# Optimization experiments

Hardware: AMD Instinct MI355X
Metric: run time of the kernel (lower is better)

## Reference

```python
import jax, jax.numpy as jnp
import numpy as np

NUM_CLASSES = 32
SIGMA = 0.02
LOG_SIGMA = float(np.log(SIGMA))
HALF_LOG_2PI = float(0.5 * np.log(2.0 * np.pi))


def _gcn(x, adj, W1, b1, W2, b2):
    # Two-layer GCN: h = relu(A x W1 + b1); out = A h W2 + b2
    h = jax.nn.relu(jnp.einsum('bij,bjf->bif', adj, x) @ W1 + b1)
    return jnp.einsum('bij,bjf->bif', adj, h) @ W2 + b2


def setup_inputs() -> dict:
    key = jax.random.key(0)
    ks = jax.random.split(key, 10)
    B, N, F = 64, 1024, 512
    x = jax.random.normal(ks[0], (B, N, F), dtype=jnp.float32)
    adj = jax.random.uniform(ks[1], (B, N, N), dtype=jnp.float32) / N  # row-scaled dense adjacency
    masks = jax.random.randint(ks[2], (B, N, F), 0, 2, dtype=jnp.int32)
    noise = jax.random.normal(ks[3], (B, N, F), dtype=jnp.float32)
    s = 0.05
    We1 = jax.random.normal(ks[4], (F, 30), dtype=jnp.float32) * s
    be1 = jnp.zeros((30,), dtype=jnp.float32)
    We2 = jax.random.normal(ks[5], (30, 18), dtype=jnp.float32) * s
    be2 = jnp.zeros((18,), dtype=jnp.float32)
    Wd1 = jax.random.normal(ks[6], (18, 30), dtype=jnp.float32) * s
    bd1 = jnp.zeros((30,), dtype=jnp.float32)
    Wd2 = jax.random.normal(ks[7], (30, F), dtype=jnp.float32) * s
    bd2 = jnp.zeros((F,), dtype=jnp.float32)
    return dict(x=x, adj=adj, masks=masks, noise=noise, We1=We1, be1=be1,
                We2=We2, be2=be2, Wd1=Wd1, bd1=bd1, Wd2=Wd2, bd2=bd2)


def reference(x, adj, masks, noise, We1, be1, We2, be2, Wd1, bd1, Wd2, bd2):
    enc = _gcn(x, adj, We1, be1, We2, be2)            # [B,N,18]
    dec = _gcn(enc, adj, Wd1, bd1, Wd2, bd2)          # [B,N,F]
    dec_act = jnp.concatenate(
        (jax.nn.softmax(dec[..., :NUM_CLASSES], axis=-1),
         jax.nn.sigmoid(dec[..., NUM_CLASSES:])), axis=-1)
    m = masks.astype(dec_act.dtype)
    # Vectorized masked reparameterized Gaussian sample: s = mu + sigma*eps
    sampled = dec_act + m * (SIGMA * noise)
    # log N(s; mu, sigma) = -eps^2/2 - log(sigma) - 0.5*log(2pi), summed over masked entries
    lp_elem = -0.5 * noise * noise - LOG_SIGMA - HALF_LOG_2PI
    log_probs = jnp.sum(m * lp_elem, axis=(1, 2))      # [B]
    return dec, sampled, log_probs
```

## Files before the change

kernel.cpp:

```cpp
#include <hip/hip_runtime.h>

#define B_ 64
#define NN 1024
#define FF 512

typedef float  fx4 __attribute__((ext_vector_type(4)));
typedef float  fx2 __attribute__((ext_vector_type(2)));
typedef int    ix4 __attribute__((ext_vector_type(4)));
typedef unsigned int   ux4i __attribute__((ext_vector_type(4)));
typedef unsigned int   ux2i __attribute__((ext_vector_type(2)));
typedef unsigned short us4  __attribute__((ext_vector_type(4)));
typedef short  sx8 __attribute__((ext_vector_type(8)));

#define FP8_SCALE   16384.0f
#define INV_SCALE   6.103515625e-5f

static __device__ __forceinline__ unsigned short f2bf(float f){
    union { float f; unsigned u; } v; v.f = f;
    unsigned r = v.u + 0x7FFFu + ((v.u >> 16) & 1u);
    return (unsigned short)(r >> 16);
}
static __device__ __forceinline__ float bf2f(unsigned short h){
    union { unsigned u; float f; } v; v.u = ((unsigned)h) << 16;
    return v.f;
}
static __device__ __forceinline__ unsigned cvt_pk_bf16(float lo, float hi){
    unsigned r;
    asm("v_cvt_pk_bf16_f32 %0, %1, %2" : "=v"(r) : "v"(lo), "v"(hi));
    return r;
}
static __device__ __forceinline__ sx8 pack_bf16x8(fx4 v0, fx4 v1){
    union { unsigned u[4]; sx8 s; } r;
    r.u[0] = cvt_pk_bf16(v0[0], v0[1]);
    r.u[1] = cvt_pk_bf16(v0[2], v0[3]);
    r.u[2] = cvt_pk_bf16(v1[0], v1[1]);
    r.u[3] = cvt_pk_bf16(v1[2], v1[3]);
    return r.s;
}
template<typename T>
static __device__ __forceinline__ T ntload(const T* p){ return __builtin_nontemporal_load(p); }
static __device__ __forceinline__ void ntstore4(float* p, fx4 v){
    __builtin_nontemporal_store(v, (fx4*)p);
}

__global__ __launch_bounds__(512) void k_xw1(
    const float* __restrict__ x, const float* __restrict__ We1,
    unsigned short* __restrict__ u1T){
    __shared__ unsigned short wls[32*512];
    int tid = threadIdx.x;
    for (int i = tid; i < 32*512; i += 512){
        int col = i >> 9, k = i & 511;
        float v = (col < 30) ? We1[k*30 + col] : 0.f;
        wls[col*512 + ((((k >> 3) ^ (col & 7)) << 3) | (k & 7))] = f2bf(v);
    }
    __syncthreads();
    int w = tid >> 6, l = tid & 63;
    int lr = l & 15, kq = l >> 4;
    int b = blockIdx.y;
    int rowb = blockIdx.x*128 + w*16;
    const float* xp = x + ((size_t)b*NN + rowb + lr)*FF + kq*8;
    fx4 acc0 = {0,0,0,0}, acc1 = {0,0,0,0};
    int c0 = lr, c1 = 16 + lr;
    #pragma unroll 4
    for (int kk = 0; kk < FF; kk += 32){
        fx4 v0 = ntload((const fx4*)(xp + kk));
        fx4 v1 = ntload((const fx4*)(xp + kk + 4));
        sx8 a = pack_bf16x8(v0, v1);
        int chunk = (kk >> 3) + kq;
        sx8 b0 = *(const sx8*)(wls + c0*512 + ((chunk ^ (c0 & 7)) << 3));
        sx8 b1 = *(const sx8*)(wls + c1*512 + ((chunk ^ (c1 & 7)) << 3));
        acc0 = __builtin_amdgcn_mfma_f32_16x16x32_bf16(a, b0, acc0, 0, 0, 0);
        acc1 = __builtin_amdgcn_mfma_f32_16x16x32_bf16(a, b1, acc1, 0, 0, 0);
    }
    int row0 = rowb + kq*4;
    us4 o0 = { f2bf(acc0[0]), f2bf(acc0[1]), f2bf(acc0[2]), f2bf(acc0[3]) };
    us4 o1 = { f2bf(acc1[0]), f2bf(acc1[1]), f2bf(acc1[2]), f2bf(acc1[3]) };
    *(us4*)(u1T + ((size_t)b*32 + c0)*NN + row0) = o0;
    *(us4*)(u1T + ((size_t)b*32 + c1)*NN + row0) = o1;
}

__global__ __launch_bounds__(256) void k_cvt_h1(
    const float* __restrict__ adjf, unsigned char* __restrict__ adj8,
    const unsigned short* __restrict__ uT, const float* __restrict__ bias,
    unsigned short* __restrict__ outT){
    __shared__ unsigned short uts[32*NN];
    int tid = threadIdx.x;
    int rt = blockIdx.x, b = blockIdx.y;
    const ux4i* src = (const ux4i*)(uT + (size_t)b*32*NN);
    #pragma unroll
    for (int i = 0; i < 16; i++){
        int j = tid + i*256;
        int c = j >> 7;
        ux4i v = src[j];
        int dst = (j*16) ^ ((c & 7) << 4);
        *(ux4i*)((char*)uts + dst) = v;
    }
    __syncthreads();
    int w = tid >> 6, l = tid & 63;
    int lr = l & 15, lk = (l >> 4) * 8;
    size_t aoff = (size_t)b*NN*NN + (size_t)(rt*128 + w*32 + lr)*NN + lk;
    int c0 = lr, c1 = 16 + lr;
    fx4 acc00 = {0,0,0,0}, acc01 = {0,0,0,0}, acc10 = {0,0,0,0}, acc11 = {0,0,0,0};
    #pragma unroll 4
    for (int kk = 0; kk < NN; kk += 32){
        fx4 v00 = ntload((const fx4*)(adjf + aoff + kk));
        fx4 v01 = ntload((const fx4*)(adjf + aoff + kk + 4));
        fx4 v10 = ntload((const fx4*)(adjf + aoff + 16*NN + kk));
        fx4 v11 = ntload((const fx4*)(adjf + aoff + 16*NN + kk + 4));
        sx8 a0 = pack_bf16x8(v00, v01);
        sx8 a1 = pack_bf16x8(v10, v11);
        {
            const float S = FP8_SCALE;
            int d0 = __builtin_amdgcn_cvt_pk_fp8_f32(v00[0]*S, v00[1]*S, 0, false);
            d0     = __builtin_amdgcn_cvt_pk_fp8_f32(v00[2]*S, v00[3]*S, d0, true);
            int d1 = __builtin_amdgcn_cvt_pk_fp8_f32(v01[0]*S, v01[1]*S, 0, false);
            d1     = __builtin_amdgcn_cvt_pk_fp8_f32(v01[2]*S, v01[3]*S, d1, true);
            ux2i s0 = { (unsigned)d0, (unsigned)d1 };
            *(ux2i*)(adj8 + aoff + kk) = s0;
            int d2 = __builtin_amdgcn_cvt_pk_fp8_f32(v10[0]*S, v10[1]*S, 0, false);
            d2     = __builtin_amdgcn_cvt_pk_fp8_f32(v10[2]*S, v10[3]*S, d2, true);
            int d3 = __builtin_amdgcn_cvt_pk_fp8_f32(v11[0]*S, v11[1]*S, 0, false);
            d3     = __builtin_amdgcn_cvt_pk_fp8_f32(v11[2]*S, v11[3]*S, d3, true);
            ux2i s1 = { (unsigned)d2, (unsigned)d3 };
            *(ux2i*)(adj8 + aoff + 16*NN + kk) = s1;
        }
        int kb = (kk + lk) * 2;
        sx8 b0 = *(const sx8*)((const char*)uts + ((c0*2048 + kb) ^ ((c0 & 7) << 4)));
        sx8 b1 = *(const sx8*)((const char*)uts + ((c1*2048 + kb) ^ ((c1 & 7) << 4)));
        acc00 = __builtin_amdgcn_mfma_f32_16x16x32_bf16(a0, b0, acc00, 0, 0, 0);
        acc01 = __builtin_amdgcn_mfma_f32_16x16x32_bf16(a0, b1, acc01, 0, 0, 0);
        acc10 = __builtin_amdgcn_mfma_f32_16x16x32_bf16(a1, b0, acc10, 0, 0, 0);
        acc11 = __builtin_amdgcn_mfma_f32_16x16x32_bf16(a1, b1, acc11, 0, 0, 0);
    }
    float bias0 = (c0 < 30) ? bias[c0] : 0.f;
    float bias1 = 0.f;
    if (c1 < 30) bias1 = bias[c1];
    int lq = l >> 4;
    #pragma unroll
    for (int mt = 0; mt < 2; mt++){
        int row0 = rt*128 + w*32 + mt*16 + lq*4;
        fx4 am0 = mt ? acc10 : acc00;
        fx4 am1 = mt ? acc11 : acc01;
        #pragma unroll
        for (int ct = 0; ct < 2; ct++){
            fx4 a = ct ? am1 : am0;
            float bb = ct ? bias1 : bias0;
            int col = ct ? c1 : c0;
            us4 o;
            #pragma unroll
            for (int j = 0; j < 4; j++){
                float v = fmaxf(a[j] + bb, 0.f);
                o[j] = f2bf(v);
            }
            *(us4*)(outT + ((size_t)b*32 + col)*NN + row0) = o;
        }
    }
}

template<int RM>
__global__ __launch_bounds__(256) void k_adjf8(
    const unsigned char* __restrict__ adj8,
    const unsigned short* __restrict__ uT,
    const float* __restrict__ bias, int biasN, float oscale,
    unsigned short* __restrict__ outT){
    __shared__ unsigned short uts[32*NN];
    int tid = threadIdx.x;
    int rt = blockIdx.x, b = blockIdx.y;
    const ux4i* src = (const ux4i*)(uT + (size_t)b*32*NN);
    #pragma unroll
    for (int i = 0; i < 16; i++){
        int j = tid + i*256;
        int c = j >> 7;
        ux4i v = src[j];
        int dst = (j*16) ^ ((c & 7) << 4);
        *(ux4i*)((char*)uts + dst) = v;
    }
    __syncthreads();
    int w = tid >> 6, l = tid & 63;
    int lr = l & 15, lk = (l >> 4) * 8;
    size_t aoff = (size_t)b*NN*NN + (size_t)(rt*128 + w*32 + lr)*NN + lk;
    int c0 = lr, c1 = 16 + lr;
    fx4 acc00 = {0,0,0,0}, acc01 = {0,0,0,0}, acc10 = {0,0,0,0}, acc11 = {0,0,0,0};
    #pragma unroll 4
    for (int kk = 0; kk < NN; kk += 32){
        ux2i q0 = *(const ux2i*)(adj8 + aoff + kk);
        ux2i q1 = *(const ux2i*)(adj8 + aoff + 16*NN + kk);
        fx2 f0 = __builtin_amdgcn_cvt_pk_f32_fp8((int)q0[0], false);
        fx2 f1 = __builtin_amdgcn_cvt_pk_f32_fp8((int)q0[0], true);
        fx2 f2 = __builtin_amdgcn_cvt_pk_f32_fp8((int)q0[1], false);
        fx2 f3 = __builtin_amdgcn_cvt_pk_f32_fp8((int)q0[1], true);
        fx2 g0 = __builtin_amdgcn_cvt_pk_f32_fp8((int)q1[0], false);
        fx2 g1 = __builtin_amdgcn_cvt_pk_f32_fp8((int)q1[0], true);
        fx2 g2 = __builtin_amdgcn_cvt_pk_f32_fp8((int)q1[1], false);
        fx2 g3 = __builtin_amdgcn_cvt_pk_f32_fp8((int)q1[1], true);
        union { unsigned u[4]; sx8 s; } A0, A1;
        A0.u[0] = cvt_pk_bf16(f0[0], f0[1]);
        A0.u[1] = cvt_pk_bf16(f1[0], f1[1]);
        A0.u[2] = cvt_pk_bf16(f2[0], f2[1]);
        A0.u[3] = cvt_pk_bf16(f3[0], f3[1]);
        A1.u[0] = cvt_pk_bf16(g0[0], g0[1]);
        A1.u[1] = cvt_pk_bf16(g1[0], g1[1]);
        A1.u[2] = cvt_pk_bf16(g2[0], g2[1]);
        A1.u[3] = cvt_pk_bf16(g3[0], g3[1]);
        int kb = (kk + lk) * 2;
        sx8 b0 = *(const sx8*)((const char*)uts + ((c0*2048 + kb) ^ ((c0 & 7) << 4)));
        sx8 b1 = *(const sx8*)((const char*)uts + ((c1*2048 + kb) ^ ((c1 & 7) << 4)));
        acc00 = __builtin_amdgcn_mfma_f32_16x16x32_bf16(A0.s, b0, acc00, 0, 0, 0);
        acc01 = __builtin_amdgcn_mfma_f32_16x16x32_bf16(A0.s, b1, acc01, 0, 0, 0);
        acc10 = __builtin_amdgcn_mfma_f32_16x16x32_bf16(A1.s, b0, acc10, 0, 0, 0);
        acc11 = __builtin_amdgcn_mfma_f32_16x16x32_bf16(A1.s, b1, acc11, 0, 0, 0);
    }
    float bias0 = 0.f, bias1 = 0.f;
    if (bias){
        if (c0 < biasN) bias0 = bias[c0];
        if (c1 < biasN) bias1 = bias[c1];
    }
    int lq = l >> 4;
    #pragma unroll
    for (int mt = 0; mt < 2; mt++){
        int row0 = rt*128 + w*32 + mt*16 + lq*4;
        fx4 am0 = mt ? acc10 : acc00;
        fx4 am1 = mt ? acc11 : acc01;
        #pragma unroll
        for (int ct = 0; ct < 2; ct++){
            fx4 a = ct ? am1 : am0;
            float bb = ct ? bias1 : bias0;
            int col = ct ? c1 : c0;
            us4 o;
            #pragma unroll
            for (int j = 0; j < 4; j++){
                float v = (a[j] + bb) * oscale;
                o[j] = f2bf(v);
            }
            if (RM){
                #pragma unroll
                for (int j = 0; j < 4; j++)
                    outT[((size_t)b*NN + row0 + j)*32 + col] = o[j];
            } else {
                *(us4*)(outT + ((size_t)b*32 + col)*NN + row0) = o;
            }
        }
    }
}

template<int JI, int CO, bool RELU>
__global__ __launch_bounds__(256) void k_tiny(
    const unsigned short* __restrict__ inT, const float* __restrict__ W,
    const float* __restrict__ bias, float oscale,
    unsigned short* __restrict__ outT){
    int n = blockIdx.x*256 + threadIdx.x;
    int b = blockIdx.y;
    const unsigned short* ip = inT + (size_t)b*32*NN + n;
    float in[JI];
    #pragma unroll
    for (int j = 0; j < JI; j++) in[j] = bf2f(ip[j*NN]);
    float acc[CO];
    #pragma unroll
    for (int c = 0; c < CO; c++) acc[c] = bias ? bias[c] : 0.f;
    #pragma unroll
    for (int j = 0; j < JI; j++){
        #pragma unroll
        for (int c = 0; c < CO; c++) acc[c] += in[j] * W[j*CO + c];
    }
    unsigned short* op = outT + (size_t)b*32*NN + n;
    #pragma unroll
    for (int c = 0; c < 32; c++){
        float v = (c < CO) ? (RELU ? fmaxf(acc[c], 0.f) : acc[c]) * oscale : 0.f;
        op[c*NN] = f2bf(v);
    }
}

__global__ __launch_bounds__(512, 2) void k_dec(
    const unsigned short* __restrict__ v2R,
    const float* __restrict__ Wd2, const float* __restrict__ bd2,
    const int* __restrict__ masks, const float* __restrict__ noise,
    float* __restrict__ dec, float* __restrict__ sampled, float* __restrict__ part){
    __shared__ unsigned short wls[512*40];
    __shared__ float dls[16][516];
    __shared__ float red[8];
    int tid = threadIdx.x;
    for (int i = tid; i < 512*32; i += 512){
        int col = i & 511, k = i >> 9;
        float v = (k < 30) ? Wd2[k*512 + col] : 0.f;
        wls[col*40 + k] = f2bf(v);
    }
    int w = tid >> 6, l = tid & 63;
    int lr = l & 15, kq = l >> 4;
    const float LPC = 2.9930844722234733f;
    float lpacc = 0.f;
    __syncthreads();
    #pragma unroll
    for (int it = 0; it < 4; it++){
        int rbase = blockIdx.x*64 + it*16;
        size_t offA = (size_t)(rbase + w)*FF + l*8;
        size_t offB = (size_t)(rbase + w + 8)*FF + l*8;
        ix4 mA0 = ntload((const ix4*)(masks + offA));
        ix4 mA1 = ntload((const ix4*)(masks + offA + 4));
        fx4 zA0 = ntload((const fx4*)(noise + offA));
        fx4 zA1 = ntload((const fx4*)(noise + offA + 4));
        ix4 mB0 = ntload((const ix4*)(masks + offB));
        ix4 mB1 = ntload((const ix4*)(masks + offB + 4));
        fx4 zB0 = ntload((const fx4*)(noise + offB));
        fx4 zB1 = ntload((const fx4*)(noise + offB + 4));
        sx8 a = *(const sx8*)(v2R + (size_t)(rbase + lr)*32 + kq*8);
        #pragma unroll
        for (int i = 0; i < 4; i++){
            int c = (w + 8*i)*16 + lr;
            sx8 bb = *(const sx8*)(wls + c*40 + kq*8);
            fx4 acc = {0,0,0,0};
            acc = __builtin_amdgcn_mfma_f32_16x16x32_bf16(a, bb, acc, 0, 0, 0);
            float bi = bd2[c];
            #pragma unroll
            for (int j = 0; j < 4; j++)
                dls[kq*4 + j][c] = acc[j] + bi;
        }
        __syncthreads();
        #pragma unroll
        for (int s = 0; s < 2; s++){
            int rloc = s ? (w + 8) : w;
            size_t off = s ? offB : offA;
            ix4 m0 = s ? mB0 : mA0;  ix4 m1 = s ? mB1 : mA1;
            fx4 z0 = s ? zB0 : zA0;  fx4 z1 = s ? zB1 : zA1;
            fx4 d0 = *(const fx4*)&dls[rloc][l*8];
            fx4 d1 = *(const fx4*)&dls[rloc][l*8 + 4];
            float av[8];
            #pragma unroll
            for (int i = 0; i < 4; i++){
                av[i]   = 1.f/(1.f + __expf(-d0[i]));
                av[4+i] = 1.f/(1.f + __expf(-d1[i]));
            }
            if (l < 4){
                float mx = d0[0];
                #pragma unroll
                for (int i = 1; i < 4; i++) mx = fmaxf(mx, d0[i]);
                #pragma unroll
                for (int i = 0; i < 4; i++) mx = fmaxf(mx, d1[i]);
                mx = fmaxf(mx, __shfl_xor(mx, 1, 4));
                mx = fmaxf(mx, __shfl_xor(mx, 2, 4));
                float e[8], ss = 0.f;
                #pragma unroll
                for (int i = 0; i < 4; i++){ e[i] = __expf(d0[i] - mx); ss += e[i]; }
                #pragma unroll
                for (int i = 0; i < 4; i++){ e[4+i] = __expf(d1[i] - mx); ss += e[4+i]; }
                ss += __shfl_xor(ss, 1, 4);
                ss += __shfl_xor(ss, 2, 4);
                float inv = 1.f / ss;
                #pragma unroll
                for (int i = 0; i < 8; i++) av[i] = e[i]*inv;
            }
            ntstore4(dec + off,     d0);
            ntstore4(dec + off + 4, d1);
            fx4 sm0, sm1;
            #pragma unroll
            for (int i = 0; i < 4; i++){
                float mi0 = (float)m0[i], zi0 = z0[i];
                float mi1 = (float)m1[i], zi1 = z1[i];
                sm0[i] = av[i]   + mi0*(0.02f*zi0);
                sm1[i] = av[4+i] + mi1*(0.02f*zi1);
                lpacc = fmaf(mi0, LPC - 0.5f*zi0*zi0, lpacc);
                lpacc = fmaf(mi1, LPC - 0.5f*zi1*zi1, lpacc);
            }
            ntstore4(sampled + off,     sm0);
            ntstore4(sampled + off + 4, sm1);
        }
        __syncthreads();
    }
    #pragma unroll
    for (int off = 32; off > 0; off >>= 1) lpacc += __shfl_xor(lpacc, off);
    if (l == 0) red[w] = lpacc;
    __syncthreads();
    if (tid == 0){
        float s = 0.f;
        #pragma unroll
        for (int i = 0; i < 8; i++) s += red[i];
        part[blockIdx.x] = s;
    }
}

__global__ void k_lp(const float* __restrict__ part, float* __restrict__ logp){
    int t = threadIdx.x;
    float s = 0.f;
    #pragma unroll
    for (int i = 0; i < 16; i++) s += part[t*16 + i];
    logp[t] = s;
}

extern "C" void kernel_launch(void* const* d_in, const int* in_sizes, int n_in,
                              void* d_out, int out_size, void* d_ws, size_t ws_size,
                              hipStream_t stream){
    const float* x     = (const float*)d_in[0];
    const float* adj   = (const float*)d_in[1];
    const int*   masks = (const int*)  d_in[2];
    const float* noise = (const float*)d_in[3];
    const float* We1   = (const float*)d_in[4];
    const float* be1   = (const float*)d_in[5];
    const float* We2   = (const float*)d_in[6];
    const float* be2   = (const float*)d_in[7];
    const float* Wd1   = (const float*)d_in[8];
    const float* bd1   = (const float*)d_in[9];
    const float* Wd2   = (const float*)d_in[10];
    const float* bd2   = (const float*)d_in[11];

    float* dec     = (float*)d_out;
    float* sampled = dec + (size_t)B_*NN*FF;
    float* logp    = sampled + (size_t)B_*NN*FF;
    unsigned char* adj8 = (unsigned char*)d_out;
    unsigned short* bufA = (unsigned short*)d_ws;
    unsigned short* bufB = bufA + (size_t)B_*32*NN;
    float* part = (float*)bufB;

    k_xw1<<<dim3(8, B_), 512, 0, stream>>>(x, We1, bufA);
    k_cvt_h1<<<dim3(8, B_), 256, 0, stream>>>(adj, adj8, bufA, be1, bufB);
    k_tiny<30,18,false><<<dim3(4, B_), 256, 0, stream>>>(bufB, We2, nullptr, INV_SCALE, bufA);
    k_adjf8<0><<<dim3(8, B_), 256, 0, stream>>>(adj8, bufA, be2, 18, INV_SCALE, bufB);
    k_adjf8<0><<<dim3(8, B_), 256, 0, stream>>>(adj8, bufB, nullptr, 0, 1.0f, bufA);
    k_tiny<18,30,true><<<dim3(4, B_), 256, 0, stream>>>(bufA, Wd1, bd1, INV_SCALE, bufB);
    k_adjf8<1><<<dim3(8, B_), 256, 0, stream>>>(adj8, bufB, nullptr, 0, 1.0f, bufA);
    k_dec<<<1024, 512, 0, stream>>>(bufA, Wd2, bd2, masks, noise, dec, sampled, part);
    k_lp<<<1, 64, 0, stream>>>(part, logp);
}
```

Baseline: 336.6 us.

## Fuse tiny GCN weight GEMMs and final adjacency GEMM into neighbouring kernels

The two small per-node dense transforms (h1·We2 and v1·Wd1) are folded into the epilogues of the adjacency-GEMM kernels, staged through shared memory, so the separate k_tiny launches and their intermediate buffer round-trips disappear. When the workspace is large enough, the FP8 adjacency copy moves to the workspace. The last adjacency GEMM is then fused with the Wd2 projection, activation, sampling and log-prob kernel, which drops one more launch and buffer pass. The fused decoder runs only 256 blocks of 512 threads with about 94 KB of shared memory each. That may leave too little parallelism to hide latency in the bandwidth-bound masks/noise/output streaming phase. A fallback path keeps the old structure when the workspace is small.

```diff
diff --git a/kernel.cpp b/kernel.cpp
--- a/kernel.cpp
+++ b/kernel.cpp
@@ -79,21 +79,23 @@
     *(us4*)(u1T + ((size_t)b*32 + c1)*NN + row0) = o1;
 }
 
-__global__ __launch_bounds__(256) void k_cvt_h1(
+__global__ __launch_bounds__(256) void k_cvt_h1u2(
     const float* __restrict__ adjf, unsigned char* __restrict__ adj8,
-    const unsigned short* __restrict__ uT, const float* __restrict__ bias,
-    unsigned short* __restrict__ outT){
+    const unsigned short* __restrict__ uT, const float* __restrict__ be1,
+    const float* __restrict__ We2, unsigned short* __restrict__ u2T){
     __shared__ unsigned short uts[32*NN];
+    __shared__ unsigned short hls[128][34];
+    __shared__ float wels[540];
     int tid = threadIdx.x;
     int rt = blockIdx.x, b = blockIdx.y;
+    for (int i = tid; i < 540; i += 256) wels[i] = We2[i];
     const ux4i* src = (const ux4i*)(uT + (size_t)b*32*NN);
     #pragma unroll
     for (int i = 0; i < 16; i++){
         int j = tid + i*256;
         int c = j >> 7;
         ux4i v = src[j];
-        int dst = (j*16) ^ ((c & 7) << 4);
-        *(ux4i*)((char*)uts + dst) = v;
+        *(ux4i*)((char*)uts + ((j*16) ^ ((c & 7) << 4))) = v;
     }
     __syncthreads();
     int w = tid >> 6, l = tid & 63;
@@ -132,13 +134,12 @@
         acc10 = __builtin_amdgcn_mfma_f32_16x16x32_bf16(a1, b0, acc10, 0, 0, 0);
         acc11 = __builtin_amdgcn_mfma_f32_16x16x32_bf16(a1, b1, acc11, 0, 0, 0);
     }
-    float bias0 = (c0 < 30) ? bias[c0] : 0.f;
-    float bias1 = 0.f;
-    if (c1 < 30) bias1 = bias[c1];
+    float bias0 = (c0 < 30) ? be1[c0] : 0.f;
+    float bias1 = (c1 < 30) ? be1[c1] : 0.f;
     int lq = l >> 4;
     #pragma unroll
     for (int mt = 0; mt < 2; mt++){
-        int row0 = rt*128 + w*32 + mt*16 + lq*4;
+        int rl0 = w*32 + mt*16 + lq*4;
         fx4 am0 = mt ? acc10 : acc00;
         fx4 am1 = mt ? acc11 : acc01;
         #pragma unroll
@@ -146,15 +147,29 @@
             fx4 a = ct ? am1 : am0;
             float bb = ct ? bias1 : bias0;
             int col = ct ? c1 : c0;
-            us4 o;
-            #pragma unroll
-            for (int j = 0; j < 4; j++){
-                float v = fmaxf(a[j] + bb, 0.f);
-                o[j] = f2bf(v);
-            }
-            *(us4*)(outT + ((size_t)b*32 + col)*NN + row0) = o;
-        }
-    }
+            #pragma unroll
+            for (int j = 0; j < 4; j++)
+                hls[rl0 + j][col] = f2bf(fmaxf(a[j] + bb, 0.f));
+        }
+    }
+    __syncthreads();
+    int row = tid >> 1, half = tid & 1;
+    float h[30];
+    #pragma unroll
+    for (int j = 0; j < 30; j++) h[j] = bf2f(hls[row][j]);
+    float acc2[9] = {0,0,0,0,0,0,0,0,0};
+    #pragma unroll
+    for (int j = 0; j < 30; j++){
+        #pragma unroll
+        for (int c = 0; c < 9; c++) acc2[c] += h[j]*wels[j*18 + half*9 + c];
+    }
+    unsigned short* base = u2T + (size_t)b*32*NN + rt*128 + row;
+    #pragma unroll
+    for (int c = 0; c < 9; c++)
+        base[(size_t)(half*9 + c)*NN] = f2bf(acc2[c]*INV_SCALE);
+    #pragma unroll
+    for (int i = 0; i < 7; i++)
+        base[(size_t)(18 + half*7 + i)*NN] = 0;
 }
 
 template<int RM>
@@ -172,8 +187,7 @@
         int j = tid + i*256;
         int c = j >> 7;
         ux4i v = src[j];
-        int dst = (j*16) ^ ((c & 7) << 4);
-        *(ux4i*)((char*)uts + dst) = v;
+        *(ux4i*)((char*)uts + ((j*16) ^ ((c & 7) << 4))) = v;
     }
     __syncthreads();
     int w = tid >> 6, l = tid & 63;
@@ -243,30 +257,264 @@
     }
 }
 
-template<int JI, int CO, bool RELU>
-__global__ __launch_bounds__(256) void k_tiny(
-    const unsigned short* __restrict__ inT, const float* __restrict__ W,
-    const float* __restrict__ bias, float oscale,
-    unsigned short* __restrict__ outT){
-    int n = blockIdx.x*256 + threadIdx.x;
-    int b = blockIdx.y;
-    const unsigned short* ip = inT + (size_t)b*32*NN + n;
-    float in[JI];
-    #pragma unroll
-    for (int j = 0; j < JI; j++) in[j] = bf2f(ip[j*NN]);
-    float acc[CO];
-    #pragma unroll
-    for (int c = 0; c < CO; c++) acc[c] = bias ? bias[c] : 0.f;
-    #pragma unroll
-    for (int j = 0; j < JI; j++){
-        #pragma unroll
-        for (int c = 0; c < CO; c++) acc[c] += in[j] * W[j*CO + c];
-    }
-    unsigned short* op = outT + (size_t)b*32*NN + n;
-    #pragma unroll
-    for (int c = 0; c < 32; c++){
-        float v = (c < CO) ? (RELU ? fmaxf(acc[c], 0.f) : acc[c]) * oscale : 0.f;
-        op[c*NN] = f2bf(v);
+__global__ __launch_bounds__(256) void k_v1h2(
+    const unsigned char* __restrict__ adj8,
+    const unsigned short* __restrict__ encT,
+    const float* __restrict__ Wd1, const float* __restrict__ bd1,
+    unsigned short* __restrict__ h2T){
+    __shared__ unsigned short uts[32*NN];
+    __shared__ unsigned short vls[128][34];
+    __shared__ float wd[540];
+    __shared__ float bdl[30];
+    int tid = threadIdx.x;
+    int rt = blockIdx.x, b = blockIdx.y;
+    for (int i = tid; i < 540; i += 256) wd[i] = Wd1[i];
+    if (tid < 30) bdl[tid] = bd1[tid];
+    const ux4i* src = (const ux4i*)(encT + (size_t)b*32*NN);
+    #pragma unroll
+    for (int i = 0; i < 16; i++){
+        int j = tid + i*256;
+        int c = j >> 7;
+        ux4i v = src[j];
+        *(ux4i*)((char*)uts + ((j*16) ^ ((c & 7) << 4))) = v;
+    }
+    __syncthreads();
+    int w = tid >> 6, l = tid & 63;
+    int lr = l & 15, lk = (l >> 4) * 8;
+    size_t aoff = (size_t)b*NN*NN + (size_t)(rt*128 + w*32 + lr)*NN + lk;
+    int c0 = lr, c1 = 16 + lr;
+    fx4 acc00 = {0,0,0,0}, acc01 = {0,0,0,0}, acc10 = {0,0,0,0}, acc11 = {0,0,0,0};
+    #pragma unroll 4
+    for (int kk = 0; kk < NN; kk += 32){
+        ux2i q0 = *(const ux2i*)(adj8 + aoff + kk);
+        ux2i q1 = *(const ux2i*)(adj8 + aoff + 16*NN + kk);
+        fx2 f0 = __builtin_amdgcn_cvt_pk_f32_fp8((int)q0[0], false);
+        fx2 f1 = __builtin_amdgcn_cvt_pk_f32_fp8((int)q0[0], true);
+        fx2 f2 = __builtin_amdgcn_cvt_pk_f32_fp8((int)q0[1], false);
+        fx2 f3 = __builtin_amdgcn_cvt_pk_f32_fp8((int)q0[1], true);
+        fx2 g0 = __builtin_amdgcn_cvt_pk_f32_fp8((int)q1[0], false);
+        fx2 g1 = __builtin_amdgcn_cvt_pk_f32_fp8((int)q1[0], true);
+        fx2 g2 = __builtin_amdgcn_cvt_pk_f32_fp8((int)q1[1], false);
+        fx2 g3 = __builtin_amdgcn_cvt_pk_f32_fp8((int)q1[1], true);
+        union { unsigned u[4]; sx8 s; } A0, A1;
+        A0.u[0] = cvt_pk_bf16(f0[0], f0[1]);
+        A0.u[1] = cvt_pk_bf16(f1[0], f1[1]);
+        A0.u[2] = cvt_pk_bf16(f2[0], f2[1]);
+        A0.u[3] = cvt_pk_bf16(f3[0], f3[1]);
+        A1.u[0] = cvt_pk_bf16(g0[0], g0[1]);
+        A1.u[1] = cvt_pk_bf16(g1[0], g1[1]);
+        A1.u[2] = cvt_pk_bf16(g2[0], g2[1]);
+        A1.u[3] = cvt_pk_bf16(g3[0], g3[1]);
+        int kb = (kk + lk) * 2;
+        sx8 b0 = *(const sx8*)((const char*)uts + ((c0*2048 + kb) ^ ((c0 & 7) << 4)));
+        sx8 b1 = *(const sx8*)((const char*)uts + ((c1*2048 + kb) ^ ((c1 & 7) << 4)));
+        acc00 = __builtin_amdgcn_mfma_f32_16x16x32_bf16(A0.s, b0, acc00, 0, 0, 0);
+        acc01 = __builtin_amdgcn_mfma_f32_16x16x32_bf16(A0.s, b1, acc01, 0, 0, 0);
+        acc10 = __builtin_amdgcn_mfma_f32_16x16x32_bf16(A1.s, b0, acc10, 0, 0, 0);
+        acc11 = __builtin_amdgcn_mfma_f32_16x16x32_bf16(A1.s, b1, acc11, 0, 0, 0);
+    }
+    int lq = l >> 4;
+    #pragma unroll
+    for (int mt = 0; mt < 2; mt++){
+        int rl0 = w*32 + mt*16 + lq*4;
+        fx4 am0 = mt ? acc10 : acc00;
+        fx4 am1 = mt ? acc11 : acc01;
+        #pragma unroll
+        for (int ct = 0; ct < 2; ct++){
+            fx4 a = ct ? am1 : am0;
+            int col = ct ? c1 : c0;
+            #pragma unroll
+            for (int j = 0; j < 4; j++)
+                vls[rl0 + j][col] = f2bf(a[j]);
+        }
+    }
+    __syncthreads();
+    int row = tid >> 1, half = tid & 1;
+    float v[18];
+    #pragma unroll
+    for (int j = 0; j < 18; j++) v[j] = bf2f(vls[row][j]);
+    float acc2[15];
+    #pragma unroll
+    for (int c = 0; c < 15; c++) acc2[c] = 0.f;
+    #pragma unroll
+    for (int j = 0; j < 18; j++){
+        #pragma unroll
+        for (int c = 0; c < 15; c++) acc2[c] += v[j]*wd[j*30 + half*15 + c];
+    }
+    unsigned short* base = h2T + (size_t)b*32*NN + rt*128 + row;
+    #pragma unroll
+    for (int c = 0; c < 15; c++){
+        int cc = half*15 + c;
+        base[(size_t)cc*NN] = f2bf(fmaxf(acc2[c] + bdl[cc], 0.f)*INV_SCALE);
+    }
+    base[(size_t)(30 + half)*NN] = 0;
+}
+
+__global__ __launch_bounds__(512) void k_v2dec(
+    const unsigned char* __restrict__ adj8,
+    const unsigned short* __restrict__ h2T,
+    const float* __restrict__ Wd2, const float* __restrict__ bd2,
+    const int* __restrict__ masks, const float* __restrict__ noise,
+    float* __restrict__ dec, float* __restrict__ sampled, float* __restrict__ part){
+    __shared__ __align__(16) char smem[94464];
+    __shared__ float red[8];
+    unsigned short* uts = (unsigned short*)smem;
+    unsigned short* wls = (unsigned short*)smem;
+    float (*dls)[516]   = (float(*)[516])(smem + 40960);
+    unsigned short* v2ls = (unsigned short*)(smem + 73984);
+    int tid = threadIdx.x;
+    int rt = blockIdx.x, b = blockIdx.y;
+    int w = tid >> 6, l = tid & 63;
+    int lr = l & 15, kq = l >> 4, lk = kq*8;
+    const ux4i* src = (const ux4i*)(h2T + (size_t)b*32*NN);
+    #pragma unroll
+    for (int i = 0; i < 8; i++){
+        int j = tid + i*512;
+        int c = j >> 7;
+        ux4i v = src[j];
+        *(ux4i*)((char*)uts + ((j*16) ^ ((c & 7) << 4))) = v;
+    }
+    __syncthreads();
+    size_t aoff = (size_t)b*NN*NN + (size_t)(rt*256 + w*32 + lr)*NN + lk;
+    int c0 = lr, c1 = 16 + lr;
+    fx4 acc00 = {0,0,0,0}, acc01 = {0,0,0,0}, acc10 = {0,0,0,0}, acc11 = {0,0,0,0};
+    #pragma unroll 4
+    for (int kk = 0; kk < NN; kk += 32){
+        ux2i q0 = *(const ux2i*)(adj8 + aoff + kk);
+        ux2i q1 = *(const ux2i*)(adj8 + aoff + 16*NN + kk);
+        fx2 f0 = __builtin_amdgcn_cvt_pk_f32_fp8((int)q0[0], false);
+        fx2 f1 = __builtin_amdgcn_cvt_pk_f32_fp8((int)q0[0], true);
+        fx2 f2 = __builtin_amdgcn_cvt_pk_f32_fp8((int)q0[1], false);
+        fx2 f3 = __builtin_amdgcn_cvt_pk_f32_fp8((int)q0[1], true);
+        fx2 g0 = __builtin_amdgcn_cvt_pk_f32_fp8((int)q1[0], false);
+        fx2 g1 = __builtin_amdgcn_cvt_pk_f32_fp8((int)q1[0], true);
+        fx2 g2 = __builtin_amdgcn_cvt_pk_f32_fp8((int)q1[1], false);
+        fx2 g3 = __builtin_amdgcn_cvt_pk_f32_fp8((int)q1[1], true);
+        union { unsigned u[4]; sx8 s; } A0, A1;
+        A0.u[0] = cvt_pk_bf16(f0[0], f0[1]);
+        A0.u[1] = cvt_pk_bf16(f1[0], f1[1]);
+        A0.u[2] = cvt_pk_bf16(f2[0], f2[1]);
+        A0.u[3] = cvt_pk_bf16(f3[0], f3[1]);
+        A1.u[0] = cvt_pk_bf16(g0[0], g0[1]);
+        A1.u[1] = cvt_pk_bf16(g1[0], g1[1]);
+        A1.u[2] = cvt_pk_bf16(g2[0], g2[1]);
+        A1.u[3] = cvt_pk_bf16(g3[0], g3[1]);
+        int kb = (kk + lk) * 2;
+        sx8 b0 = *(const sx8*)((const char*)uts + ((c0*2048 + kb) ^ ((c0 & 7) << 4)));
+        sx8 b1 = *(const sx8*)((const char*)uts + ((c1*2048 + kb) ^ ((c1 & 7) << 4)));
+        acc00 = __builtin_amdgcn_mfma_f32_16x16x32_bf16(A0.s, b0, acc00, 0, 0, 0);
+        acc01 = __builtin_amdgcn_mfma_f32_16x16x32_bf16(A0.s, b1, acc01, 0, 0, 0);
+        acc10 = __builtin_amdgcn_mfma_f32_16x16x32_bf16(A1.s, b0, acc10, 0, 0, 0);
+        acc11 = __builtin_amdgcn_mfma_f32_16x16x32_bf16(A1.s, b1, acc11, 0, 0, 0);
+    }
+    #pragma unroll
+    for (int mt = 0; mt < 2; mt++){
+        int rl0 = w*32 + mt*16 + kq*4;
+        fx4 am0 = mt ? acc10 : acc00;
+        fx4 am1 = mt ? acc11 : acc01;
+        #pragma unroll
+        for (int ct = 0; ct < 2; ct++){
+            fx4 a = ct ? am1 : am0;
+            int col = ct ? c1 : c0;
+            #pragma unroll
+            for (int j = 0; j < 4; j++)
+                v2ls[(rl0 + j)*40 + col] = f2bf(a[j]);
+        }
+    }
+    __syncthreads();
+    for (int i = tid; i < 512*32; i += 512){
+        int col = i & 511, k = i >> 9;
+        float v = (k < 30) ? Wd2[k*512 + col] : 0.f;
+        wls[col*40 + k] = f2bf(v);
+    }
+    __syncthreads();
+    const float LPC = 2.9930844722234733f;
+    float lpacc = 0.f;
+    int growbase = b*NN + rt*256;
+    for (int it = 0; it < 16; it++){
+        int rb = it*16;
+        size_t offA = (size_t)(growbase + rb + w)*FF + l*8;
+        size_t offB = offA + (size_t)8*FF;
+        ix4 mA0 = ntload((const ix4*)(masks + offA));
+        ix4 mA1 = ntload((const ix4*)(masks + offA + 4));
+        fx4 zA0 = ntload((const fx4*)(noise + offA));
+        fx4 zA1 = ntload((const fx4*)(noise + offA + 4));
+        ix4 mB0 = ntload((const ix4*)(masks + offB));
+        ix4 mB1 = ntload((const ix4*)(masks + offB + 4));
+        fx4 zB0 = ntload((const fx4*)(noise + offB));
+        fx4 zB1 = ntload((const fx4*)(noise + offB + 4));
+        sx8 a = *(const sx8*)(v2ls + (rb + lr)*40 + kq*8);
+        #pragma unroll
+        for (int i = 0; i < 4; i++){
+            int c = (w + 8*i)*16 + lr;
+            sx8 bb = *(const sx8*)(wls + c*40 + kq*8);
+            fx4 acc = {0,0,0,0};
+            acc = __builtin_amdgcn_mfma_f32_16x16x32_bf16(a, bb, acc, 0, 0, 0);
+            float bi = bd2[c];
+            #pragma unroll
+            for (int j = 0; j < 4; j++)
+                dls[kq*4 + j][c] = acc[j] + bi;
+        }
+        __syncthreads();
+        #pragma unroll
+        for (int s = 0; s < 2; s++){
+            int rloc = s ? (w + 8) : w;
+            size_t off = s ? offB : offA;
+            ix4 m0 = s ? mB0 : mA0;  ix4 m1 = s ? mB1 : mA1;
+            fx4 z0 = s ? zB0 : zA0;  fx4 z1 = s ? zB1 : zA1;
+            fx4 d0 = *(const fx4*)&dls[rloc][l*8];
+            fx4 d1 = *(const fx4*)&dls[rloc][l*8 + 4];
+            float av[8];
+            #pragma unroll
+            for (int i = 0; i < 4; i++){
+                av[i]   = 1.f/(1.f + __expf(-d0[i]));
+                av[4+i] = 1.f/(1.f + __expf(-d1[i]));
+            }
+            if (l < 4){
+                float mx = d0[0];
+                #pragma unroll
+                for (int i = 1; i < 4; i++) mx = fmaxf(mx, d0[i]);
+                #pragma unroll
+                for (int i = 0; i < 4; i++) mx = fmaxf(mx, d1[i]);
+                mx = fmaxf(mx, __shfl_xor(mx, 1, 4));
+                mx = fmaxf(mx, __shfl_xor(mx, 2, 4));
+                float e[8], ss = 0.f;
+                #pragma unroll
+                for (int i = 0; i < 4; i++){ e[i] = __expf(d0[i] - mx); ss += e[i]; }
+                #pragma unroll
+                for (int i = 0; i < 4; i++){ e[4+i] = __expf(d1[i] - mx); ss += e[4+i]; }
+                ss += __shfl_xor(ss, 1, 4);
+                ss += __shfl_xor(ss, 2, 4);
+                float inv = 1.f / ss;
+                #pragma unroll
+                for (int i = 0; i < 8; i++) av[i] = e[i]*inv;
+            }
+            ntstore4(dec + off,     d0);
+            ntstore4(dec + off + 4, d1);
+            fx4 sm0, sm1;
+            #pragma unroll
+            for (int i = 0; i < 4; i++){
+                float mi0 = (float)m0[i], zi0 = z0[i];
+                float mi1 = (float)m1[i], zi1 = z1[i];
+                sm0[i] = av[i]   + mi0*(0.02f*zi0);
+                sm1[i] = av[4+i] + mi1*(0.02f*zi1);
+                lpacc = fmaf(mi0, LPC - 0.5f*zi0*zi0, lpacc);
+                lpacc = fmaf(mi1, LPC - 0.5f*zi1*zi1, lpacc);
+            }
+            ntstore4(sampled + off,     sm0);
+            ntstore4(sampled + off + 4, sm1);
+        }
+        __syncthreads();
+    }
+    #pragma unroll
+    for (int off = 32; off > 0; off >>= 1) lpacc += __shfl_xor(lpacc, off);
+    if (l == 0) red[w] = lpacc;
+    __syncthreads();
+    if (tid == 0){
+        float s = 0.f;
+        #pragma unroll
+        for (int i = 0; i < 8; i++) s += red[i];
+        part[blockIdx.y*4 + blockIdx.x] = s;
     }
 }
 
@@ -377,11 +625,12 @@
     }
 }
 
+template<int PB>
 __global__ void k_lp(const float* __restrict__ part, float* __restrict__ logp){
     int t = threadIdx.x;
     float s = 0.f;
     #pragma unroll
-    for (int i = 0; i < 16; i++) s += part[t*16 + i];
+    for (int i = 0; i < PB; i++) s += part[t*PB + i];
     logp[t] = s;
 }
 
@@ -404,18 +653,36 @@
     float* dec     = (float*)d_out;
     float* sampled = dec + (size_t)B_*NN*FF;
     float* logp    = sampled + (size_t)B_*NN*FF;
-    unsigned char* adj8 = (unsigned char*)d_out;
-    unsigned short* bufA = (unsigned short*)d_ws;
-    unsigned short* bufB = bufA + (size_t)B_*32*NN;
-    float* part = (float*)bufB;
+
+    const size_t ADJ8_BYTES = (size_t)B_*NN*NN;
+    const size_t BUF_ELEMS  = (size_t)B_*32*NN;
+    bool bigws = ws_size >= ADJ8_BYTES + 4*BUF_ELEMS + 1024;
+
+    unsigned char* adj8;
+    unsigned short *bufA, *bufB;
+    if (bigws){
+        adj8 = (unsigned char*)d_ws;
+        bufA = (unsigned short*)((char*)d_ws + ADJ8_BYTES);
+        bufB = bufA + BUF_ELEMS;
+    } else {
+        adj8 = (unsigned char*)d_out;
+        bufA = (unsigned short*)d_ws;
+        bufB = bufA + BUF_ELEMS;
+    }
 
     k_xw1<<<dim3(8, B_), 512, 0, stream>>>(x, We1, bufA);
-    k_cvt_h1<<<dim3(8, B_), 256, 0, stream>>>(adj, adj8, bufA, be1, bufB);
-    k_tiny<30,18,false><<<dim3(4, B_), 256, 0, stream>>>(bufB, We2, nullptr, INV_SCALE, bufA);
-    k_adjf8<0><<<dim3(8, B_), 256, 0, stream>>>(adj8, bufA, be2, 18, INV_SCALE, bufB);
-    k_adjf8<0><<<dim3(8, B_), 256, 0, stream>>>(adj8, bufB, nullptr, 0, 1.0f, bufA);
-    k_tiny<18,30,true><<<dim3(4, B_), 256, 0, stream>>>(bufA, Wd1, bd1, INV_SCALE, bufB);
-    k_adjf8<1><<<dim3(8, B_), 256, 0, stream>>>(adj8, bufB, nullptr, 0, 1.0f, bufA);
-    k_dec<<<1024, 512, 0, stream>>>(bufA, Wd2, bd2, masks, noise, dec, sampled, part);
-    k_lp<<<1, 64, 0, stream>>>(part, logp);
-}
+    k_cvt_h1u2<<<dim3(8, B_), 256, 0, stream>>>(adj, adj8, bufA, be1, We2, bufB);
+    k_adjf8<0><<<dim3(8, B_), 256, 0, stream>>>(adj8, bufB, be2, 18, INV_SCALE, bufA);
+    k_v1h2<<<dim3(8, B_), 256, 0, stream>>>(adj8, bufA, Wd1, bd1, bufB);
+    if (bigws){
+        float* part = (float*)bufA;
+        k_v2dec<<<dim3(4, B_), 512, 0, stream>>>(adj8, bufB, Wd2, bd2, masks, noise,
+                                                 dec, sampled, part);
+        k_lp<4><<<1, 64, 0, stream>>>(part, logp);
+    } else {
+        float* part = (float*)bufB;
+        k_adjf8<1><<<dim3(8, B_), 256, 0, stream>>>(adj8, bufB, nullptr, 0, 1.0f, bufA);
+        k_dec<<<1024, 512, 0, stream>>>(bufA, Wd2, bd2, masks, noise, dec, sampled, part);
+        k_lp<16><<<1, 64, 0, stream>>>(part, logp);
+    }
+}
```

Result: faster. 328.7 us (-2.3%).
